# Optimization experiments

Measured on AMD Instinct MI355X. Metric: run time of the kernel, lower is better.

## Reference

```python
import jax, jax.numpy as jnp
import numpy as np

TAU = 1.0            # temperature (self.temperature.item())
FAST_WEIGHT_DECAY = 0.01
FAST_WEIGHT_LR = 0.01

B, IN, H = 128, 1024, 1024


def setup_inputs() -> dict:
    key = jax.random.key(0)
    k = jax.random.split(key, 6)
    scale_ih = 1.0 / np.sqrt(IN)
    scale_hh = np.sqrt(2.0 / (H + H))  # xavier_uniform-like std
    return {
        "x_t": jax.random.normal(k[0], (B, IN), jnp.float32),
        "h_prev": jax.random.normal(k[1], (B, H), jnp.float32),
        "W_ih": jax.random.normal(k[2], (H, IN), jnp.float32) * scale_ih,
        "b_ih": jnp.zeros((H,), jnp.float32),
        "W_hh_fixed": jax.random.normal(k[3], (H, H), jnp.float32) * scale_hh,
        "W_hh_virtual": jnp.zeros((H, H), jnp.float32),
        "gumbel_u": jax.random.uniform(k[4], (B, H, H), jnp.float32),
    }


def reference(x_t, h_prev, W_ih, b_ih, W_hh_fixed, W_hh_virtual, gumbel_u):
    # input contribution: Linear(input_size, hidden_size)
    input_contrib = x_t @ W_ih.T + b_ih                      # (B, H)

    # logits scaled by temperature once, then gumbel_softmax divides by tau again
    logits = (W_hh_fixed + W_hh_virtual) / TAU               # (H, H)
    eps = 1e-9
    g = -jnp.log(-jnp.log(jnp.clip(gumbel_u, eps, 1.0 - eps)))  # Gumbel(0,1), (B,H,H)
    y = jax.nn.softmax((logits[None, :, :] + g) / TAU, axis=2)  # soft sampling, (B,H,H)

    # weighted exchange: each output neuron o reduces sampled weights against h_prev
    contrib = jnp.einsum('boh,bh->bo', y, h_prev)            # (B, H)
    h_next = jnp.tanh(input_contrib + contrib)               # (B, H)

    # Hebbian fast-weight update (no_grad in original)
    hebbian = jnp.einsum('bo,bh->oh', h_next, h_prev) / B    # mean over batch, (H,H)
    W_hh_virtual_new = jax.lax.stop_gradient(
        W_hh_virtual * (1.0 - FAST_WEIGHT_DECAY) + hebbian * FAST_WEIGHT_LR
    )
    return h_next, W_hh_virtual_new
```

## Files before the change

kernel.cpp:

```cpp
#include <hip/hip_runtime.h>
#include <hip/hip_bf16.h>
#include <cstddef>

#define B_DIM  128
#define IN_DIM 1024
#define H_DIM  1024

constexpr float kDecay   = 1.0f - 0.01f;
constexpr float kLrOverB = 0.01f / 128.0f;

typedef float f32x4 __attribute__((ext_vector_type(4)));

__global__ __launch_bounds__(256) void input_gemm(
    const float* __restrict__ x_t,
    const float* __restrict__ W_ih,
    const float* __restrict__ b_ih,
    float* __restrict__ ic)
{
    const int o0 = blockIdx.x * 64;
    const int b0 = blockIdx.y * 16;
    const int t  = threadIdx.x;

    __shared__ float Wt[64][68];
    __shared__ float xs[64][17];

    const int tx = t & 15;
    const int ty = t >> 4;

    float acc[4] = {0.f, 0.f, 0.f, 0.f};

    for (int kc = 0; kc < IN_DIM / 64; ++kc) {
        const int k0 = kc * 64;

#pragma unroll
        for (int ii = 0; ii < 4; ++ii) {
            const int i  = t + 256 * ii;
            const int r  = i >> 4;
            const int c4 = (i & 15) * 4;
            const float4 wv = *reinterpret_cast<const float4*>(
                &W_ih[(size_t)(o0 + r) * IN_DIM + k0 + c4]);
            Wt[c4 + 0][r] = wv.x; Wt[c4 + 1][r] = wv.y;
            Wt[c4 + 2][r] = wv.z; Wt[c4 + 3][r] = wv.w;
        }
        {
            const int br = t >> 4;
            const int c4 = (t & 15) * 4;
            const float4 xv = *reinterpret_cast<const float4*>(
                &x_t[(size_t)(b0 + br) * IN_DIM + k0 + c4]);
            xs[c4 + 0][br] = xv.x; xs[c4 + 1][br] = xv.y;
            xs[c4 + 2][br] = xv.z; xs[c4 + 3][br] = xv.w;
        }
        __syncthreads();

#pragma unroll 8
        for (int k = 0; k < 64; ++k) {
            const float  xb = xs[k][ty];
            const float4 wv = *reinterpret_cast<const float4*>(&Wt[k][4 * tx]);
            acc[0] = fmaf(wv.x, xb, acc[0]);
            acc[1] = fmaf(wv.y, xb, acc[1]);
            acc[2] = fmaf(wv.z, xb, acc[2]);
            acc[3] = fmaf(wv.w, xb, acc[3]);
        }
        __syncthreads();
    }

    const int o = o0 + 4 * tx;
    const int b = b0 + ty;
    float4 r;
    r.x = acc[0] + b_ih[o + 0];
    r.y = acc[1] + b_ih[o + 1];
    r.z = acc[2] + b_ih[o + 2];
    r.w = acc[3] + b_ih[o + 3];
    *reinterpret_cast<float4*>(&ic[(size_t)b * H_DIM + o]) = r;
}

__global__ __launch_bounds__(256, 3) void fused_rows(
    const float* __restrict__ h_prev,
    const float* __restrict__ W_f,
    const float* __restrict__ W_v,
    const float* __restrict__ gu,
    const float* __restrict__ ic,
    float* __restrict__ h_next)
{
    const int b0 = blockIdx.x * 4;
    const int o0 = blockIdx.y * 8;
    const int t  = threadIdx.x;
    const int w  = t >> 6, lane = t & 63;

    __shared__ __align__(16) float e_s[8 * H_DIM];

    {
        const float4* f4 = reinterpret_cast<const float4*>(W_f) + (size_t)o0 * 256;
        const float4* v4 = reinterpret_cast<const float4*>(W_v) + (size_t)o0 * 256;
        float4*       dst = reinterpret_cast<float4*>(e_s);
#pragma unroll
        for (int ii = 0; ii < 8; ++ii) {
            const float4 a = f4[t + 256 * ii];
            const float4 b = v4[t + 256 * ii];
            float4 ee;
            ee.x = __expf(a.x + b.x); ee.y = __expf(a.y + b.y);
            ee.z = __expf(a.z + b.z); ee.w = __expf(a.w + b.w);
            dst[t + 256 * ii] = ee;
        }
    }
    __syncthreads();

    const int b = b0 + w;

    const float4* hp4 = reinterpret_cast<const float4*>(h_prev + (size_t)b * H_DIM);
    float4 p[4];
#pragma unroll
    for (int j = 0; j < 4; ++j) p[j] = hp4[lane + 64 * j];

    const f32x4*  g4 = reinterpret_cast<const f32x4*>(gu)
                     + ((size_t)b * H_DIM + o0) * 256;
    const float4* e4 = reinterpret_cast<const float4*>(e_s);

    f32x4 ug[4][4];
    float s[8], d[8];

#pragma unroll
    for (int tp = 0; tp < 4; ++tp)
#pragma unroll
        for (int j = 0; j < 4; ++j)
            ug[tp][j] = __builtin_nontemporal_load(g4 + tp * 256 + lane + 64 * j);

#pragma unroll
    for (int oi = 0; oi < 8; ++oi) {
        const int sl = oi & 3;

        float sum = 0.f, dot = 0.f;
#pragma unroll
        for (int j = 0; j < 4; ++j) {
            const f32x4  uu = ug[sl][j];
            const float4 ee = e4[oi * 256 + lane + 64 * j];
            const float4 pp = p[j];
            const float q0 = __fdividef(ee.x, -__log2f(fmaxf(uu.x, 1e-9f)));
            const float q1 = __fdividef(ee.y, -__log2f(fmaxf(uu.y, 1e-9f)));
            const float q2 = __fdividef(ee.z, -__log2f(fmaxf(uu.z, 1e-9f)));
            const float q3 = __fdividef(ee.w, -__log2f(fmaxf(uu.w, 1e-9f)));
            sum += (q0 + q1) + (q2 + q3);
            dot = fmaf(q0, pp.x, dot);
            dot = fmaf(q1, pp.y, dot);
            dot = fmaf(q2, pp.z, dot);
            dot = fmaf(q3, pp.w, dot);
        }
        s[oi] = sum;
        d[oi] = dot;

        if (oi < 4) {
            const f32x4* gn = g4 + (size_t)(oi + 4) * 256;
#pragma unroll
            for (int j = 0; j < 4; ++j)
                ug[sl][j] = __builtin_nontemporal_load(gn + lane + 64 * j);
        }
    }

#pragma unroll
    for (int off = 32; off > 0; off >>= 1) {
#pragma unroll
        for (int r = 0; r < 8; ++r) {
            s[r] += __shfl_xor(s[r], off, 64);
            d[r] += __shfl_xor(d[r], off, 64);
        }
    }

    if (lane == 0) {
        const size_t base = (size_t)b * H_DIM + o0;
        const float4 i0 = *reinterpret_cast<const float4*>(ic + base);
        const float4 i1 = *reinterpret_cast<const float4*>(ic + base + 4);
        float4 r0, r1;
        r0.x = tanhf(i0.x + __fdividef(d[0], s[0]));
        r0.y = tanhf(i0.y + __fdividef(d[1], s[1]));
        r0.z = tanhf(i0.z + __fdividef(d[2], s[2]));
        r0.w = tanhf(i0.w + __fdividef(d[3], s[3]));
        r1.x = tanhf(i1.x + __fdividef(d[4], s[4]));
        r1.y = tanhf(i1.y + __fdividef(d[5], s[5]));
        r1.z = tanhf(i1.z + __fdividef(d[6], s[6]));
        r1.w = tanhf(i1.w + __fdividef(d[7], s[7]));
        *reinterpret_cast<float4*>(h_next + base)     = r0;
        *reinterpret_cast<float4*>(h_next + base + 4) = r1;
    }
}

__global__ __launch_bounds__(256) void hebbian_update(
    const float* __restrict__ h_next,
    const float* __restrict__ h_prev,
    const float* __restrict__ W_v,
    float* __restrict__ W_out)
{
    const int h0 = blockIdx.x * 64;
    const int o0 = blockIdx.y * 64;
    const int t  = threadIdx.x;

    __shared__ __align__(16) float hn_s[B_DIM][64];
    __shared__ __align__(16) float hp_s[B_DIM][64];

#pragma unroll
    for (int i = 0; i < 32; ++i) {
        const int e  = t + 256 * i;
        const int bb = e >> 6;
        const int cc = e & 63;
        hn_s[bb][cc] = h_next[(size_t)bb * H_DIM + o0 + cc];
        hp_s[bb][cc] = h_prev[(size_t)bb * H_DIM + h0 + cc];
    }
    __syncthreads();

    const int tx = t & 15;
    const int ty = t >> 4;

    float acc[4][4] = {{0.f}};

#pragma unroll 8
    for (int b = 0; b < B_DIM; ++b) {
        const float4 av = reinterpret_cast<const float4*>(hn_s[b])[ty];
        const float4 bv = reinterpret_cast<const float4*>(hp_s[b])[tx];
        const float aa[4] = {av.x, av.y, av.z, av.w};
        const float bb[4] = {bv.x, bv.y, bv.z, bv.w};
#pragma unroll
        for (int a = 0; a < 4; ++a)
#pragma unroll
            for (int c = 0; c < 4; ++c)
                acc[a][c] = fmaf(aa[a], bb[c], acc[a][c]);
    }

#pragma unroll
    for (int a = 0; a < 4; ++a) {
        const int o = o0 + 4 * ty + a;
        const size_t base = (size_t)o * H_DIM + h0 + 4 * tx;
        const float4 wv = *reinterpret_cast<const float4*>(W_v + base);
        float4 r;
        r.x = wv.x * kDecay + acc[a][0] * kLrOverB;
        r.y = wv.y * kDecay + acc[a][1] * kLrOverB;
        r.z = wv.z * kDecay + acc[a][2] * kLrOverB;
        r.w = wv.w * kDecay + acc[a][3] * kLrOverB;
        *reinterpret_cast<float4*>(W_out + base) = r;
    }
}

extern "C" void kernel_launch(void* const* d_in, const int* in_sizes, int n_in,
                              void* d_out, int out_size, void* d_ws, size_t ws_size,
                              hipStream_t stream)
{
    const float* x_t    = (const float*)d_in[0];
    const float* h_prev = (const float*)d_in[1];
    const float* W_ih   = (const float*)d_in[2];
    const float* b_ih   = (const float*)d_in[3];
    const float* W_f    = (const float*)d_in[4];
    const float* W_v    = (const float*)d_in[5];
    const float* gu     = (const float*)d_in[6];

    float* out    = (float*)d_out;
    float* h_next = out;
    float* W_out  = out + (size_t)B_DIM * H_DIM;

    float* ic = (float*)d_ws;

    input_gemm<<<dim3(H_DIM / 64, B_DIM / 16), 256, 0, stream>>>(
        x_t, W_ih, b_ih, ic);

    fused_rows<<<dim3(B_DIM / 4, H_DIM / 8), 256, 0, stream>>>(
        h_prev, W_f, W_v, gu, ic, h_next);

    hebbian_update<<<dim3(H_DIM / 64, H_DIM / 64), 256, 0, stream>>>(
        h_next, h_prev, W_v, W_out);
}
```

Measured before the change: 145.5 us.

## Stream gumbel rows through LDS ring via direct global-to-LDS loads

Replaces the register-held nontemporal prefetch of four gumbel rows with a per-wave double-buffered LDS ring filled by global_load_lds, using explicit vmcnt waits to pipeline row loads against compute. This is meant to free VGPRs and keep the memory stream overlapped with the log/divide work. In exchange it adds 32KB of LDS per block, drops the occupancy hint from 3 to 2, and reduces the prefetch depth from four rows to two. The new LDS reads also add an LDS access per element, and there is no barrier between the ring reads and the refill of the same slot, which relies on in-order wave execution.

```diff
diff --git a/kernel.cpp b/kernel.cpp
--- a/kernel.cpp
+++ b/kernel.cpp
@@ -9,7 +9,13 @@
 constexpr float kDecay   = 1.0f - 0.01f;
 constexpr float kLrOverB = 0.01f / 128.0f;
 
-typedef float f32x4 __attribute__((ext_vector_type(4)));
+__device__ __forceinline__ void gload_lds16(const float* g, float* l)
+{
+    __builtin_amdgcn_global_load_lds(
+        (const __attribute__((address_space(1))) void*)g,
+        (__attribute__((address_space(3))) void*)l,
+        16, 0, 0);
+}
 
 __global__ __launch_bounds__(256) void input_gemm(
     const float* __restrict__ x_t,
@@ -74,7 +80,7 @@
     *reinterpret_cast<float4*>(&ic[(size_t)b * H_DIM + o]) = r;
 }
 
-__global__ __launch_bounds__(256, 3) void fused_rows(
+__global__ __launch_bounds__(256, 2) void fused_rows(
     const float* __restrict__ h_prev,
     const float* __restrict__ W_f,
     const float* __restrict__ W_v,
@@ -88,6 +94,7 @@
     const int w  = t >> 6, lane = t & 63;
 
     __shared__ __align__(16) float e_s[8 * H_DIM];
+    __shared__ __align__(16) float ring[4][2][1024];
 
     {
         const float4* f4 = reinterpret_cast<const float4*>(W_f) + (size_t)o0 * 256;
@@ -112,27 +119,38 @@
 #pragma unroll
     for (int j = 0; j < 4; ++j) p[j] = hp4[lane + 64 * j];
 
-    const f32x4*  g4 = reinterpret_cast<const f32x4*>(gu)
-                     + ((size_t)b * H_DIM + o0) * 256;
-    const float4* e4 = reinterpret_cast<const float4*>(e_s);
-
-    f32x4 ug[4][4];
+    asm volatile("s_waitcnt vmcnt(0)" ::: "memory");
+    __builtin_amdgcn_sched_barrier(0);
+
+    const float* grow = gu + ((size_t)b * H_DIM + o0) * H_DIM;
+    const float4* e4  = reinterpret_cast<const float4*>(e_s);
+
+#pragma unroll
+    for (int j = 0; j < 4; ++j)
+        gload_lds16(grow + 0 * 1024 + j * 256 + lane * 4, &ring[w][0][j * 256]);
+#pragma unroll
+    for (int j = 0; j < 4; ++j)
+        gload_lds16(grow + 1 * 1024 + j * 256 + lane * 4, &ring[w][1][j * 256]);
+
     float s[8], d[8];
 
 #pragma unroll
-    for (int tp = 0; tp < 4; ++tp)
-#pragma unroll
-        for (int j = 0; j < 4; ++j)
-            ug[tp][j] = __builtin_nontemporal_load(g4 + tp * 256 + lane + 64 * j);
-
-#pragma unroll
     for (int oi = 0; oi < 8; ++oi) {
-        const int sl = oi & 3;
+        const int slot = oi & 1;
+
+        if (oi < 7) {
+            asm volatile("s_waitcnt vmcnt(4)" ::: "memory");
+        } else {
+            asm volatile("s_waitcnt vmcnt(0)" ::: "memory");
+        }
+        __builtin_amdgcn_sched_barrier(0);
+
+        const float4* tile4 = reinterpret_cast<const float4*>(ring[w][slot]);
 
         float sum = 0.f, dot = 0.f;
 #pragma unroll
         for (int j = 0; j < 4; ++j) {
-            const f32x4  uu = ug[sl][j];
+            const float4 uu = tile4[lane + 64 * j];
             const float4 ee = e4[oi * 256 + lane + 64 * j];
             const float4 pp = p[j];
             const float q0 = __fdividef(ee.x, -__log2f(fmaxf(uu.x, 1e-9f)));
@@ -148,11 +166,11 @@
         s[oi] = sum;
         d[oi] = dot;
 
-        if (oi < 4) {
-            const f32x4* gn = g4 + (size_t)(oi + 4) * 256;
+        if (oi < 6) {
+            const float* gn = grow + (size_t)(oi + 2) * 1024;
 #pragma unroll
             for (int j = 0; j < 4; ++j)
-                ug[sl][j] = __builtin_nontemporal_load(gn + lane + 64 * j);
+                gload_lds16(gn + j * 256 + lane * 4, &ring[w][slot][j * 256]);
         }
     }
 
```

New measurement: 175.1 us. +20.3%, slower.

## Amortize exp(W) staging across 16 batch rows per block in fused_rows

Applied to the files above, without the earlier changes.

Each fused_rows block now processes 16 batch rows instead of 4, reusing the exp(W_f+W_v) tile staged in LDS across four passes. This cuts the redundant global reads and exp work for the 8x1024 weight slice by four. Gumbel loads are double-buffered with two slots, continuing across batch iterations, and h_prev for the next row is prefetched. Occupancy hint rises to 4 blocks/SM, grid shrinks fourfold, which may reduce latency hiding on the streaming gumbel read.

```diff
diff --git a/kernel.cpp b/kernel.cpp
--- a/kernel.cpp
+++ b/kernel.cpp
@@ -74,7 +74,7 @@
     *reinterpret_cast<float4*>(&ic[(size_t)b * H_DIM + o]) = r;
 }
 
-__global__ __launch_bounds__(256, 3) void fused_rows(
+__global__ __launch_bounds__(256, 4) void fused_rows(
     const float* __restrict__ h_prev,
     const float* __restrict__ W_f,
     const float* __restrict__ W_v,
@@ -82,8 +82,8 @@
     const float* __restrict__ ic,
     float* __restrict__ h_next)
 {
-    const int b0 = blockIdx.x * 4;
-    const int o0 = blockIdx.y * 8;
+    const int o0 = blockIdx.x * 8;
+    const int b0 = blockIdx.y * 16;
     const int t  = threadIdx.x;
     const int w  = t >> 6, lane = t & 63;
 
@@ -105,81 +105,108 @@
     }
     __syncthreads();
 
-    const int b = b0 + w;
-
-    const float4* hp4 = reinterpret_cast<const float4*>(h_prev + (size_t)b * H_DIM);
-    float4 p[4];
-#pragma unroll
-    for (int j = 0; j < 4; ++j) p[j] = hp4[lane + 64 * j];
-
-    const f32x4*  g4 = reinterpret_cast<const f32x4*>(gu)
-                     + ((size_t)b * H_DIM + o0) * 256;
     const float4* e4 = reinterpret_cast<const float4*>(e_s);
-
-    f32x4 ug[4][4];
-    float s[8], d[8];
-
-#pragma unroll
-    for (int tp = 0; tp < 4; ++tp)
+    const int bA = b0 + w;
+
+    float4 pc[4], pn[4];
+    {
+        const float4* hp4 = reinterpret_cast<const float4*>(h_prev + (size_t)bA * H_DIM);
+#pragma unroll
+        for (int j = 0; j < 4; ++j) pc[j] = hp4[lane + 64 * j];
+    }
+
+    f32x4 ug[2][4];
+
+    {
+        const f32x4* g0 = reinterpret_cast<const f32x4*>(gu)
+                        + ((size_t)bA * H_DIM + o0) * 256;
 #pragma unroll
         for (int j = 0; j < 4; ++j)
-            ug[tp][j] = __builtin_nontemporal_load(g4 + tp * 256 + lane + 64 * j);
-
-#pragma unroll
-    for (int oi = 0; oi < 8; ++oi) {
-        const int sl = oi & 3;
-
-        float sum = 0.f, dot = 0.f;
-#pragma unroll
-        for (int j = 0; j < 4; ++j) {
-            const f32x4  uu = ug[sl][j];
-            const float4 ee = e4[oi * 256 + lane + 64 * j];
-            const float4 pp = p[j];
-            const float q0 = __fdividef(ee.x, -__log2f(fmaxf(uu.x, 1e-9f)));
-            const float q1 = __fdividef(ee.y, -__log2f(fmaxf(uu.y, 1e-9f)));
-            const float q2 = __fdividef(ee.z, -__log2f(fmaxf(uu.z, 1e-9f)));
-            const float q3 = __fdividef(ee.w, -__log2f(fmaxf(uu.w, 1e-9f)));
-            sum += (q0 + q1) + (q2 + q3);
-            dot = fmaf(q0, pp.x, dot);
-            dot = fmaf(q1, pp.y, dot);
-            dot = fmaf(q2, pp.z, dot);
-            dot = fmaf(q3, pp.w, dot);
-        }
-        s[oi] = sum;
-        d[oi] = dot;
-
-        if (oi < 4) {
-            const f32x4* gn = g4 + (size_t)(oi + 4) * 256;
-#pragma unroll
-            for (int j = 0; j < 4; ++j)
-                ug[sl][j] = __builtin_nontemporal_load(gn + lane + 64 * j);
-        }
-    }
-
-#pragma unroll
-    for (int off = 32; off > 0; off >>= 1) {
-#pragma unroll
-        for (int r = 0; r < 8; ++r) {
-            s[r] += __shfl_xor(s[r], off, 64);
-            d[r] += __shfl_xor(d[r], off, 64);
-        }
-    }
-
-    if (lane == 0) {
-        const size_t base = (size_t)b * H_DIM + o0;
-        const float4 i0 = *reinterpret_cast<const float4*>(ic + base);
-        const float4 i1 = *reinterpret_cast<const float4*>(ic + base + 4);
-        float4 r0, r1;
-        r0.x = tanhf(i0.x + __fdividef(d[0], s[0]));
-        r0.y = tanhf(i0.y + __fdividef(d[1], s[1]));
-        r0.z = tanhf(i0.z + __fdividef(d[2], s[2]));
-        r0.w = tanhf(i0.w + __fdividef(d[3], s[3]));
-        r1.x = tanhf(i1.x + __fdividef(d[4], s[4]));
-        r1.y = tanhf(i1.y + __fdividef(d[5], s[5]));
-        r1.z = tanhf(i1.z + __fdividef(d[6], s[6]));
-        r1.w = tanhf(i1.w + __fdividef(d[7], s[7]));
-        *reinterpret_cast<float4*>(h_next + base)     = r0;
-        *reinterpret_cast<float4*>(h_next + base + 4) = r1;
+            ug[0][j] = __builtin_nontemporal_load(g0 + lane + 64 * j);
+#pragma unroll
+        for (int j = 0; j < 4; ++j)
+            ug[1][j] = __builtin_nontemporal_load(g0 + 256 + lane + 64 * j);
+    }
+
+#pragma unroll
+    for (int k = 0; k < 4; ++k) {
+        const int b = bA + 4 * k;
+        const f32x4* gk  = reinterpret_cast<const f32x4*>(gu)
+                         + ((size_t)b * H_DIM + o0) * 256;
+        const f32x4* gk1 = reinterpret_cast<const f32x4*>(gu)
+                         + ((size_t)(b + 4) * H_DIM + o0) * 256;
+
+        float s[8], d[8];
+
+#pragma unroll
+        for (int oi = 0; oi < 8; ++oi) {
+            const int slot = oi & 1;
+
+            float sum = 0.f, dot = 0.f;
+#pragma unroll
+            for (int j = 0; j < 4; ++j) {
+                const f32x4  uu = ug[slot][j];
+                const float4 ee = e4[oi * 256 + lane + 64 * j];
+                const float4 pp = pc[j];
+                const float q0 = __fdividef(ee.x, -__log2f(fmaxf(uu.x, 1e-9f)));
+                const float q1 = __fdividef(ee.y, -__log2f(fmaxf(uu.y, 1e-9f)));
+                const float q2 = __fdividef(ee.z, -__log2f(fmaxf(uu.z, 1e-9f)));
+                const float q3 = __fdividef(ee.w, -__log2f(fmaxf(uu.w, 1e-9f)));
+                sum += (q0 + q1) + (q2 + q3);
+                dot = fmaf(q0, pp.x, dot);
+                dot = fmaf(q1, pp.y, dot);
+                dot = fmaf(q2, pp.z, dot);
+                dot = fmaf(q3, pp.w, dot);
+            }
+            s[oi] = sum;
+            d[oi] = dot;
+
+            if (k < 3 || oi < 6) {
+                const f32x4* gsrc = (oi < 6) ? (gk + (size_t)(oi + 2) * 256)
+                                             : (gk1 + (size_t)(oi - 6) * 256);
+#pragma unroll
+                for (int j = 0; j < 4; ++j)
+                    ug[slot][j] = __builtin_nontemporal_load(gsrc + lane + 64 * j);
+            }
+
+            if (oi == 3 && k < 3) {
+                const float4* hpn = reinterpret_cast<const float4*>(
+                    h_prev + (size_t)(b + 4) * H_DIM);
+#pragma unroll
+                for (int j = 0; j < 4; ++j) pn[j] = hpn[lane + 64 * j];
+            }
+        }
+
+#pragma unroll
+        for (int off = 32; off > 0; off >>= 1) {
+#pragma unroll
+            for (int r = 0; r < 8; ++r) {
+                s[r] += __shfl_xor(s[r], off, 64);
+                d[r] += __shfl_xor(d[r], off, 64);
+            }
+        }
+
+        if (lane == 0) {
+            const size_t base = (size_t)b * H_DIM + o0;
+            const float4 i0 = *reinterpret_cast<const float4*>(ic + base);
+            const float4 i1 = *reinterpret_cast<const float4*>(ic + base + 4);
+            float4 r0, r1;
+            r0.x = tanhf(i0.x + __fdividef(d[0], s[0]));
+            r0.y = tanhf(i0.y + __fdividef(d[1], s[1]));
+            r0.z = tanhf(i0.z + __fdividef(d[2], s[2]));
+            r0.w = tanhf(i0.w + __fdividef(d[3], s[3]));
+            r1.x = tanhf(i1.x + __fdividef(d[4], s[4]));
+            r1.y = tanhf(i1.y + __fdividef(d[5], s[5]));
+            r1.z = tanhf(i1.z + __fdividef(d[6], s[6]));
+            r1.w = tanhf(i1.w + __fdividef(d[7], s[7]));
+            *reinterpret_cast<float4*>(h_next + base)     = r0;
+            *reinterpret_cast<float4*>(h_next + base + 4) = r1;
+        }
+
+        if (k < 3) {
+#pragma unroll
+            for (int j = 0; j < 4; ++j) pc[j] = pn[j];
+        }
     }
 }
 
@@ -259,7 +286,7 @@
     input_gemm<<<dim3(H_DIM / 64, B_DIM / 16), 256, 0, stream>>>(
         x_t, W_ih, b_ih, ic);
 
-    fused_rows<<<dim3(B_DIM / 4, H_DIM / 8), 256, 0, stream>>>(
+    fused_rows<<<dim3(H_DIM / 8, B_DIM / 16), 256, 0, stream>>>(
         h_prev, W_f, W_v, gu, ic, h_next);
 
     hebbian_update<<<dim3(H_DIM / 64, H_DIM / 64), 256, 0, stream>>>(
```

After: 137.2 us. 1.06x faster.
